# Kernel tuning notes

Hardware: AMD Instinct MI355X
Metric: run time of the kernel (lower is better)

## Reference

```python
import jax, jax.numpy as jnp
import numpy as np

B, C, H, N, K = 512, 256, 1024, 500000, 5

_PARAM_DIMS = [("w_in", C, H), ("w_h1", H, H), ("w_s2", H, H), ("w_s3", H, H),
               ("w_h2", H, H), ("w_s1o", H, H), ("w_s2o", H, H), ("w_h3", H, H),
               ("w_mu", H, C), ("w_s", H, C)]


def setup_inputs() -> dict:
    key = jax.random.key(0)
    inp = {}
    k_codes, k_book, k_params = jax.random.split(key, 3)
    inp["codes"] = jax.random.normal(k_codes, (B, C), dtype=jnp.float32)
    inp["codebook"] = jax.random.normal(k_book, (N, C), dtype=jnp.float32)
    ks = jax.random.split(k_params, len(_PARAM_DIMS))
    for (name, fin, fout), k in zip(_PARAM_DIMS, ks):
        k1, k2 = jax.random.split(k)
        s = 1.0 / np.sqrt(fin)
        inp[name] = jax.random.uniform(k1, (fout, fin), minval=-s, maxval=s, dtype=jnp.float32)
        inp["b" + name[1:]] = jax.random.uniform(k2, (fout,), minval=-s, maxval=s, dtype=jnp.float32)
    return inp


def _linear(x, w, b):
    # torch nn.Linear: x @ W^T + b, W is [out, in]
    return x @ w.T + b


def _encode(prev, w_in, b_in, w_h1, b_h1, w_s2, b_s2, w_s3, b_s3,
            w_h2, b_h2, w_s1o, b_s1o, w_s2o, b_s2o, w_h3, b_h3,
            w_mu, b_mu, w_s, b_s):
    i = jnp.tanh(_linear(prev, w_in, b_in))
    h1 = jnp.tanh(_linear(i, w_h1, b_h1))
    s2 = jnp.tanh(_linear(h1, w_s2, b_s2))
    s3 = jnp.tanh(_linear(h1, w_s3, b_s3))
    h2 = jnp.tanh(_linear(h1 + s2, w_h2, b_h2))
    o1 = jnp.tanh(_linear(h1, w_s1o, b_s1o))
    o2 = jnp.tanh(_linear(h2, w_s2o, b_s2o))
    o3 = jnp.tanh(_linear(h2 + s3, w_h3, b_h3))
    out = o1 + o2 + o3
    return _linear(out, w_mu, b_mu), _linear(out, w_s, b_s)


def reference(codes, codebook, w_in, b_in, w_h1, b_h1, w_s2, b_s2, w_s3, b_s3,
              w_h2, b_h2, w_s1o, b_s1o, w_s2o, b_s2o, w_h3, b_h3,
              w_mu, b_mu, w_s, b_s):
    # flat k-NN search: squared L2 dists via the matmul expansion
    codes2 = jnp.sum(codebook * codebook, axis=1)                      # [N]
    dists = (-2.0 * (codes @ codebook.T)
             + jnp.sum(codes * codes, axis=1, keepdims=True)
             + codes2[None, :])                                        # [B, N]
    neg_d, nbrs = jax.lax.top_k(-dists, K)                             # smallest K
    # eval mode: chosen_neighbor_index = 0 -> nearest neighbor
    prev = codebook[nbrs[:, 0]]                                        # [B, C]
    mu, logstd = _encode(prev, w_in, b_in, w_h1, b_h1, w_s2, b_s2, w_s3, b_s3,
                         w_h2, b_h2, w_s1o, b_s1o, w_s2o, b_s2o, w_h3, b_h3,
                         w_mu, b_mu, w_s, b_s)
    return (mu, logstd)
```

## Files before the change

kernel.cpp:

```cpp
#include <hip/hip_runtime.h>
#include <math.h>

#define QTOT   512
#define CDIM   256
#define HDIM   1024
#define NROWS  500000
#define NB     128
#define NTILES ((NROWS + NB - 1) / NB)
#define NPADR  (NTILES * NB)
#define LDB    264
#define DELTA  2.0f

#define C0_T   1954
#define C1_T   (NTILES - C0_T)
#define C0_R   (C0_T * NB)
#define C1_R   (C1_T * NB)

typedef short bf16x8 __attribute__((ext_vector_type(8)));
typedef float f32x4  __attribute__((ext_vector_type(4)));
typedef unsigned int u32;

__device__ __forceinline__ unsigned short bf16_rne(float f) {
  unsigned u = __float_as_uint(f);
  u += 0x7FFFu + ((u >> 16) & 1u);
  return (unsigned short)(u >> 16);
}
__device__ __forceinline__ unsigned bfp2(float a, float b) {
  return (unsigned)bf16_rne(a) | ((unsigned)bf16_rne(b) << 16);
}

__device__ __forceinline__ void gld16(const void* g, void* l) {
  __builtin_amdgcn_global_load_lds((const __attribute__((address_space(1))) u32*)g,
                                   (__attribute__((address_space(3))) u32*)l, 16, 0, 0);
}

#define FMIN_DPP(x, ctrl) do { \
    int _t = __builtin_amdgcn_update_dpp(__float_as_int(x), __float_as_int(x), (ctrl), 0xF, 0xF, false); \
    x = fminf(x, __int_as_float(_t)); } while (0)
#define FADD_DPP(x, ctrl) do { \
    int _t = __builtin_amdgcn_update_dpp(__float_as_int(x), __float_as_int(x), (ctrl), 0xF, 0xF, false); \
    x += __int_as_float(_t); } while (0)

__global__ void k_prep(const float* __restrict__ codes, unsigned short* __restrict__ a0s) {
  int q = blockIdx.x, k = threadIdx.x;
  float v = -2.0f * codes[q * CDIM + k];
  int qb = q >> 7, row = q & 127, m = row >> 4, l15 = row & 15;
  int ks = k >> 5, kin = k & 31, quad = kin >> 3, off = kin & 7;
  int lane = quad * 16 + l15;
  a0s[(((qb * 8 + m) * 8 + ks) * 64 + lane) * 8 + off] = bf16_rne(v);
}

__global__ __launch_bounds__(256) void k_conv(
    const float* __restrict__ cb, unsigned short* __restrict__ cbh,
    float* __restrict__ c2, int row0, int nrows)
{
  const int lane = threadIdx.x & 63;
  const int wid  = (blockIdx.x * 256 + threadIdx.x) >> 6;
  const int nw   = (gridDim.x * 256) >> 6;
  for (int r = wid; r < nrows; r += nw) {
    const int gr = row0 + r;
    float4 v = make_float4(0.f, 0.f, 0.f, 0.f);
    if (gr < NROWS) v = *(const float4*)(cb + (size_t)gr * CDIM + lane * 4);
    float sq = v.x * v.x + v.y * v.y + v.z * v.z + v.w * v.w;
    FADD_DPP(sq, 0xB1);
    FADD_DPP(sq, 0x4E);
    FADD_DPP(sq, 0x124);
    FADD_DPP(sq, 0x128);
    sq += __shfl_xor(sq, 16);
    sq += __shfl_xor(sq, 32);
    uint2 p; p.x = bfp2(v.x, v.y); p.y = bfp2(v.z, v.w);
    *(uint2*)((char*)cbh + (size_t)r * 512 + lane * 8) = p;
    if (lane == 0) c2[r] = (gr < NROWS) ? sq : 1e30f;
  }
}

__global__ __launch_bounds__(256, 2) void k_coarse(
    const unsigned short* __restrict__ a0s,
    const unsigned short* __restrict__ cbh,
    const float* __restrict__ c2arr,
    float* __restrict__ tileMin, int nt0)
{
  __shared__ __align__(16) unsigned short Bsh[128 * 256];
  __shared__ float c2sh[128];
  __shared__ float redf[512 * 2];

  const int tid  = threadIdx.x;
  const int lane = tid & 63;
  const int w    = tid >> 6;
  const int quad = lane >> 4;
  const int l15  = lane & 15;

  const int ntl  = blockIdx.x;
  const int ntg  = nt0 + ntl;

  const int wq = (w >> 1) * 64;
  const int wn = (w & 1) * 64;

  {
    const char* tbase = (const char*)cbh + (size_t)ntl * 65536;
#pragma unroll
    for (int i2 = 0; i2 < 16; ++i2) {
      const int i   = w * 16 + i2;
      const int row = 2 * i + (lane >> 5);
      const int cS  = lane & 31;
      gld16(tbase + (size_t)row * 512 + ((cS ^ (row & 7)) << 4),
            (char*)Bsh + i * 1024);
    }
  }
  if (tid < 128) c2sh[tid] = c2arr[ntl * NB + tid];
  __syncthreads();

  float cadd[4];
#pragma unroll
  for (int j2 = 0; j2 < 4; ++j2) cadd[j2] = c2sh[wn + j2 * 16 + l15];

  for (int qb = 0; qb < 4; ++qb) {
    const unsigned short* abase = a0s + (size_t)(qb * 8 + (w >> 1) * 4) * 4096 + lane * 8;

    f32x4 acc[4][4];
#pragma unroll
    for (int m = 0; m < 4; ++m)
#pragma unroll
      for (int j2 = 0; j2 < 4; ++j2) acc[m][j2] = (f32x4){0.f, 0.f, 0.f, 0.f};

    bf16x8 apf[3][4];
#pragma unroll
    for (int m = 0; m < 4; ++m) apf[0][m] = *(const bf16x8*)(abase + (m * 8 + 0) * 512);
#pragma unroll
    for (int m = 0; m < 4; ++m) apf[1][m] = *(const bf16x8*)(abase + (m * 8 + 1) * 512);

#pragma unroll
    for (int ks = 0; ks < 8; ++ks) {
      if (ks + 2 < 8) {
#pragma unroll
        for (int m = 0; m < 4; ++m)
          apf[(ks + 2) % 3][m] = *(const bf16x8*)(abase + (m * 8 + ks + 2) * 512);
      }
      bf16x8 b[4];
#pragma unroll
      for (int j2 = 0; j2 < 4; ++j2) {
        const int row = wn + j2 * 16 + l15;
        b[j2] = *(const bf16x8*)((const char*)Bsh + row * 512 + (((ks * 4 + quad) ^ (row & 7)) << 4));
      }
#pragma unroll
      for (int m = 0; m < 4; ++m)
#pragma unroll
        for (int j2 = 0; j2 < 4; ++j2)
          acc[m][j2] = __builtin_amdgcn_mfma_f32_16x16x32_bf16(apf[ks % 3][m], b[j2], acc[m][j2], 0, 0, 0);
    }

#pragma unroll
    for (int m = 0; m < 4; ++m) {
#pragma unroll
      for (int r = 0; r < 4; ++r) {
        float kk = fminf(fminf(acc[m][0][r] + cadd[0], acc[m][1][r] + cadd[1]),
                         fminf(acc[m][2][r] + cadd[2], acc[m][3][r] + cadd[3]));
        FMIN_DPP(kk, 0xB1);
        FMIN_DPP(kk, 0x4E);
        FMIN_DPP(kk, 0x124);
        FMIN_DPP(kk, 0x128);
        if (l15 == 0) redf[(qb * 128 + wq + m * 16 + quad * 4 + r) * 2 + (w & 1)] = kk;
      }
    }
  }
  __syncthreads();

#pragma unroll
  for (int qq = 0; qq < 2; ++qq) {
    int q = qq * 256 + tid;
    tileMin[(size_t)q * NTILES + ntg] = fminf(redf[q * 2], redf[q * 2 + 1]);
  }
}

__global__ __launch_bounds__(256, 2) void k_coarse_fb(
    const unsigned short* __restrict__ a0s,
    const float* __restrict__ cb,
    float* __restrict__ tileMin)
{
  __shared__ __align__(16) unsigned short Bsh[128 * 256];
  __shared__ float c2sh[128];
  __shared__ float redf[512 * 2];

  const int tid  = threadIdx.x;
  const int lane = tid & 63;
  const int w    = tid >> 6;
  const int quad = lane >> 4;
  const int l15  = lane & 15;

  const int nt = blockIdx.x;
  const int n0 = nt * NB;

  const int wq = (w >> 1) * 64;
  const int wn = (w & 1) * 64;

#pragma unroll 8
  for (int j = 0; j < 32; ++j) {
    int f = j * 256 + tid;
    int row = f >> 6;
    int c4  = f & 63;
    int n   = n0 + row;
    float4 v = make_float4(0.f, 0.f, 0.f, 0.f);
    if (n < NROWS) v = *(const float4*)(cb + (size_t)n * CDIM + c4 * 4);
    float sq = v.x * v.x + v.y * v.y + v.z * v.z + v.w * v.w;
    uint2 p; p.x = bfp2(v.x, v.y); p.y = bfp2(v.z, v.w);
    int chunk = (c4 >> 1) ^ (row & 7);
    *(uint2*)((char*)Bsh + row * 512 + chunk * 16 + (c4 & 1) * 8) = p;
#pragma unroll
    for (int s = 32; s; s >>= 1) sq += __shfl_xor(sq, s);
    if (lane == 0) c2sh[row] = (n < NROWS) ? sq : 1e30f;
  }
  __syncthreads();

  float cadd[4];
#pragma unroll
  for (int j2 = 0; j2 < 4; ++j2) cadd[j2] = c2sh[wn + j2 * 16 + l15];

  for (int qb = 0; qb < 4; ++qb) {
    bf16x8 afr[4][8];
    {
      const int mg0 = (w >> 1) * 4;
      const unsigned short* base = a0s + (size_t)(qb * 8 + mg0) * 8 * 64 * 8 + lane * 8;
#pragma unroll
      for (int m = 0; m < 4; ++m)
#pragma unroll
        for (int ks = 0; ks < 8; ++ks)
          afr[m][ks] = *(const bf16x8*)(base + (m * 8 + ks) * 64 * 8);
    }
    f32x4 acc[4][4];
#pragma unroll
    for (int m = 0; m < 4; ++m)
#pragma unroll
      for (int j2 = 0; j2 < 4; ++j2) acc[m][j2] = (f32x4){0.f, 0.f, 0.f, 0.f};
#pragma unroll
    for (int ks = 0; ks < 8; ++ks) {
      bf16x8 b[4];
      const int cbase = ks * 4 + quad;
#pragma unroll
      for (int j2 = 0; j2 < 4; ++j2) {
        const int row = wn + j2 * 16 + l15;
        b[j2] = *(const bf16x8*)((const char*)Bsh + row * 512 + ((cbase ^ (row & 7)) << 4));
      }
#pragma unroll
      for (int m = 0; m < 4; ++m)
#pragma unroll
        for (int j2 = 0; j2 < 4; ++j2)
          acc[m][j2] = __builtin_amdgcn_mfma_f32_16x16x32_bf16(afr[m][ks], b[j2], acc[m][j2], 0, 0, 0);
    }
#pragma unroll
    for (int m = 0; m < 4; ++m) {
#pragma unroll
      for (int r = 0; r < 4; ++r) {
        float kk = 1e30f;
#pragma unroll
        for (int j2 = 0; j2 < 4; ++j2) kk = fminf(kk, acc[m][j2][r] + cadd[j2]);
#pragma unroll
        for (int s = 1; s < 16; s <<= 1) kk = fminf(kk, __shfl_xor(kk, s));
        if (l15 == 0) redf[(qb * 128 + wq + m * 16 + quad * 4 + r) * 2 + (w & 1)] = kk;
      }
    }
  }
  __syncthreads();

#pragma unroll
  for (int qq = 0; qq < 2; ++qq) {
    int q = qq * 256 + tid;
    tileMin[(size_t)q * NTILES + nt] = fminf(redf[q * 2], redf[q * 2 + 1]);
  }
}

__global__ __launch_bounds__(256) void k_refine(
    const float* __restrict__ codes, const float* __restrict__ cb,
    const float* __restrict__ tileMin, float* __restrict__ prev)
{
#define LCAP 96
  __shared__ float csh[256];
  __shared__ float red[256];
  __shared__ int   list[LCAP];
  __shared__ int   cnt;
  __shared__ double rd[256];
  __shared__ int    rn[256];

  const int q = blockIdx.x;
  const int tid = threadIdx.x;
  csh[tid] = codes[q * CDIM + tid];
  if (tid == 0) cnt = 0;
  const float* tm = tileMin + (size_t)q * NTILES;
  float lm = 1e30f;
  for (int t = tid; t < NTILES; t += 256) lm = fminf(lm, tm[t]);
  red[tid] = lm;
  __syncthreads();
  for (int s = 128; s; s >>= 1) {
    if (tid < s) red[tid] = fminf(red[tid], red[tid + s]);
    __syncthreads();
  }
  const float thresh = red[0] + DELTA;
  for (int t = tid; t < NTILES; t += 256)
    if (tm[t] <= thresh) { int p = atomicAdd(&cnt, 1); if (p < LCAP) list[p] = t; }
  __syncthreads();
  const int nl = min(cnt, LCAP);

  double bestK = 1e300; int bestN = 0x7FFFFFFF;
  for (int li = 0; li < nl; ++li) {
    const int t = list[li];
    const int row = tid >> 1, half = tid & 1;
    const int n = t * NB + row;
    if (n < NROWS) {
      const float* r = cb + (size_t)n * CDIM;
      double dot = 0.0, sq = 0.0;
      for (int u = half * 32; u < half * 32 + 32; ++u) {
        float4 cv = *(const float4*)(r + u * 4);
        dot += (double)cv.x * csh[u*4+0] + (double)cv.y * csh[u*4+1]
             + (double)cv.z * csh[u*4+2] + (double)cv.w * csh[u*4+3];
        sq  += (double)cv.x * cv.x + (double)cv.y * cv.y
             + (double)cv.z * cv.z + (double)cv.w * cv.w;
      }
      dot += __shfl_xor(dot, 1);
      sq  += __shfl_xor(sq, 1);
      double key = sq - 2.0 * dot;
      if (key < bestK || (key == bestK && n < bestN)) { bestK = key; bestN = n; }
    }
  }
  rd[tid] = bestK; rn[tid] = bestN;
  __syncthreads();
  for (int s = 128; s; s >>= 1) {
    if (tid < s) {
      if (rd[tid + s] < rd[tid] || (rd[tid + s] == rd[tid] && rn[tid + s] < rn[tid])) {
        rd[tid] = rd[tid + s]; rn[tid] = rn[tid + s];
      }
    }
    __syncthreads();
  }
  const int nstar = rn[0];
  prev[(size_t)q * CDIM + tid] = cb[(size_t)nstar * CDIM + tid];
}

struct Job {
  const float* A1; const float* A2; const float* A3;
  const float* W;  const float* bias; float* out;
};

__global__ __launch_bounds__(256) void k_gemm(
    Job j0, Job j1, Job j2, int Kdim, int Ntot, int do_tanh)
{
  __shared__ unsigned short Ash[128 * LDB];
  __shared__ unsigned short Wsh[64 * LDB];
  __shared__ float bsh[64];

  const Job jb = (blockIdx.z == 0) ? j0 : ((blockIdx.z == 1) ? j1 : j2);
  const float* __restrict__ A1 = jb.A1;
  const float* __restrict__ A2 = jb.A2;
  const float* __restrict__ A3 = jb.A3;
  const float* __restrict__ W  = jb.W;

  const int tid  = threadIdx.x;
  const int lane = tid & 63;
  const int w    = tid >> 6;
  const int quad = lane >> 4;
  const int l15  = lane & 15;
  const int q0   = blockIdx.x * 128;
  const int n0   = blockIdx.y * 64;

  if (tid < 64) bsh[tid] = jb.bias[n0 + tid];

  f32x4 acc[2][4];
#pragma unroll
  for (int m = 0; m < 2; ++m)
#pragma unroll
    for (int j = 0; j < 4; ++j) acc[m][j] = (f32x4){0.f, 0.f, 0.f, 0.f};

  for (int kc = 0; kc < Kdim; kc += 256) {
    __syncthreads();
#pragma unroll 4
    for (int it = 0; it < 32; ++it) {
      int i = it * 256 + tid;
      int row = i >> 6, c4 = i & 63;
      size_t gi = (size_t)(q0 + row) * Kdim + kc + c4 * 4;
      float4 v = *(const float4*)(A1 + gi);
      if (A2) { float4 u = *(const float4*)(A2 + gi); v.x += u.x; v.y += u.y; v.z += u.z; v.w += u.w; }
      if (A3) { float4 u = *(const float4*)(A3 + gi); v.x += u.x; v.y += u.y; v.z += u.z; v.w += u.w; }
      uint2 p; p.x = bfp2(v.x, v.y); p.y = bfp2(v.z, v.w);
      *(uint2*)&Ash[row * LDB + c4 * 4] = p;
    }
#pragma unroll 4
    for (int it = 0; it < 16; ++it) {
      int i = it * 256 + tid;
      int row = i >> 6, c4 = i & 63;
      size_t gi = (size_t)(n0 + row) * Kdim + kc + c4 * 4;
      float4 v = *(const float4*)(W + gi);
      uint2 p; p.x = bfp2(v.x, v.y); p.y = bfp2(v.z, v.w);
      *(uint2*)&Wsh[row * LDB + c4 * 4] = p;
    }
    __syncthreads();
#pragma unroll
    for (int ks = 0; ks < 8; ++ks) {
      const int kb = ks * 32 + quad * 8;
      bf16x8 a[2], b[4];
#pragma unroll
      for (int m = 0; m < 2; ++m)
        a[m] = *(const bf16x8*)&Ash[(w * 32 + m * 16 + l15) * LDB + kb];
#pragma unroll
      for (int j = 0; j < 4; ++j)
        b[j] = *(const bf16x8*)&Wsh[(j * 16 + l15) * LDB + kb];
#pragma unroll
      for (int m = 0; m < 2; ++m)
#pragma unroll
        for (int j = 0; j < 4; ++j)
          acc[m][j] = __builtin_amdgcn_mfma_f32_16x16x32_bf16(a[m], b[j], acc[m][j], 0, 0, 0);
    }
  }

#pragma unroll
  for (int m = 0; m < 2; ++m)
#pragma unroll
    for (int j = 0; j < 4; ++j)
#pragma unroll
      for (int r = 0; r < 4; ++r) {
        int q = q0 + w * 32 + m * 16 + quad * 4 + r;
        int n = j * 16 + l15;
        float v = acc[m][j][r] + bsh[n];
        if (do_tanh) v = tanhf(v);
        jb.out[(size_t)q * Ntot + n0 + n] = v;
      }
}

extern "C" void kernel_launch(void* const* d_in, const int* in_sizes, int n_in,
                              void* d_out, int out_size, void* d_ws, size_t ws_size,
                              hipStream_t stream) {
  const float* codes = (const float*)d_in[0];
  const float* cb    = (const float*)d_in[1];
  const float* w_in  = (const float*)d_in[2];
  const float* b_in  = (const float*)d_in[3];
  const float* w_h1  = (const float*)d_in[4];
  const float* b_h1  = (const float*)d_in[5];
  const float* w_s2  = (const float*)d_in[6];
  const float* b_s2  = (const float*)d_in[7];
  const float* w_s3  = (const float*)d_in[8];
  const float* b_s3  = (const float*)d_in[9];
  const float* w_h2  = (const float*)d_in[10];
  const float* b_h2  = (const float*)d_in[11];
  const float* w_s1o = (const float*)d_in[12];
  const float* b_s1o = (const float*)d_in[13];
  const float* w_s2o = (const float*)d_in[14];
  const float* b_s2o = (const float*)d_in[15];
  const float* w_h3  = (const float*)d_in[16];
  const float* b_h3  = (const float*)d_in[17];
  const float* w_mu  = (const float*)d_in[18];
  const float* b_mu  = (const float*)d_in[19];
  const float* w_s   = (const float*)d_in[20];
  const float* b_s   = (const float*)d_in[21];
  float* out = (float*)d_out;

  char* ws = (char*)d_ws;
  unsigned short* a0s = (unsigned short*)ws;
  float* tileMin = (float*)(ws + 262144);
  float* prev    = (float*)(ws + 262144 + 8001536);
  float* acts    = (float*)(ws + 262144 + 8001536 + 524288);
  const int ACT = 512 * 1024;
  float* act_i  = acts + 0 * ACT;
  float* act_h1 = acts + 1 * ACT;
  float* act_s2 = acts + 2 * ACT;
  float* act_s3 = acts + 3 * ACT;
  float* act_h2 = acts + 4 * ACT;
  float* act_o1 = acts + 5 * ACT;
  float* act_o2 = acts + 6 * ACT;
  float* act_o3 = acts + 7 * ACT;

  const size_t CBH_OFF = 262144 + 8001536 + 524288 + 16777216;
  const size_t CBH_SZ  = (size_t)C0_R * 512;
  const size_t C2_OFF  = CBH_OFF + CBH_SZ;
  const size_t NEED    = C2_OFF + (size_t)C0_R * 4;
  unsigned short* cbh = (unsigned short*)(ws + CBH_OFF);
  float* c2buf        = (float*)(ws + C2_OFF);

  hipLaunchKernelGGL(k_prep, dim3(512), dim3(256), 0, stream, codes, a0s);

  if (ws_size >= NEED) {
    hipLaunchKernelGGL(k_conv,   dim3(2048), dim3(256), 0, stream, cb, cbh, c2buf, 0, C0_R);
    hipLaunchKernelGGL(k_coarse, dim3(C0_T), dim3(256), 0, stream, a0s, cbh, c2buf, tileMin, 0);
    hipLaunchKernelGGL(k_conv,   dim3(2048), dim3(256), 0, stream, cb, cbh, c2buf, C0_R, C1_R);
    hipLaunchKernelGGL(k_coarse, dim3(C1_T), dim3(256), 0, stream, a0s, cbh, c2buf, tileMin, C0_T);
  } else {
    hipLaunchKernelGGL(k_coarse_fb, dim3(NTILES), dim3(256), 0, stream, a0s, cb, tileMin);
  }

  hipLaunchKernelGGL(k_refine, dim3(512), dim3(256), 0, stream, codes, cb, tileMin, prev);

  const float* NUL = nullptr;
  Job in_j  = { prev,   NUL,    NUL,    w_in,  b_in,  act_i  };
  Job h1_j  = { act_i,  NUL,    NUL,    w_h1,  b_h1,  act_h1 };
  Job s2_j  = { act_h1, NUL,    NUL,    w_s2,  b_s2,  act_s2 };
  Job s3_j  = { act_h1, NUL,    NUL,    w_s3,  b_s3,  act_s3 };
  Job o1_j  = { act_h1, NUL,    NUL,    w_s1o, b_s1o, act_o1 };
  Job h2_j  = { act_h1, act_s2, NUL,    w_h2,  b_h2,  act_h2 };
  Job o2_j  = { act_h2, NUL,    NUL,    w_s2o, b_s2o, act_o2 };
  Job o3_j  = { act_h2, act_s3, NUL,    w_h3,  b_h3,  act_o3 };
  Job mu_j  = { act_o1, act_o2, act_o3, w_mu,  b_mu,  out            };
  Job ls_j  = { act_o1, act_o2, act_o3, w_s,   b_s,   out + 131072   };

  hipLaunchKernelGGL(k_gemm, dim3(4, 16, 1), dim3(256), 0, stream, in_j, in_j, in_j, 256,  1024, 1);
  hipLaunchKernelGGL(k_gemm, dim3(4, 16, 1), dim3(256), 0, stream, h1_j, h1_j, h1_j, 1024, 1024, 1);
  hipLaunchKernelGGL(k_gemm, dim3(4, 16, 3), dim3(256), 0, stream, s2_j, s3_j, o1_j, 1024, 1024, 1);
  hipLaunchKernelGGL(k_gemm, dim3(4, 16, 1), dim3(256), 0, stream, h2_j, h2_j, h2_j, 1024, 1024, 1);
  hipLaunchKernelGGL(k_gemm, dim3(4, 16, 2), dim3(256), 0, stream, o2_j, o3_j, o3_j, 1024, 1024, 1);
  hipLaunchKernelGGL(k_gemm, dim3(4, 4, 2),  dim3(256), 0, stream, mu_j, ls_j, ls_j, 1024, 256,  0);
}
```

Before: 1.332 ms.

## Persistent coarse kernel with resident query fragments and 16-row group refinement

The coarse kNN kernel becomes persistent: 256 blocks of 512 threads each keep all query A-fragments in registers and stream codebook tiles in double-buffered 64-row halves. It also records per-16-row group minima in a new workspace buffer. Refinement then rescans in fp64 only the 16-row groups under the threshold instead of whole 128-row tiles, cutting the exact rescoring work. The cost is heavy register pressure from holding 32 A fragments per thread, plus a large groupMin write (about 4000 tiles × 8 groups × 512 queries × 4 bytes) and a larger workspace requirement that may push execution onto the fallback path.

```diff
diff --git a/kernel.cpp b/kernel.cpp
--- a/kernel.cpp
+++ b/kernel.cpp
@@ -7,7 +7,7 @@
 #define NROWS  500000
 #define NB     128
 #define NTILES ((NROWS + NB - 1) / NB)
-#define NPADR  (NTILES * NB)
+#define NGRP   (NTILES * 8)
 #define LDB    264
 #define DELTA  2.0f
 
@@ -74,48 +74,76 @@
   }
 }
 
-__global__ __launch_bounds__(256, 2) void k_coarse(
+__device__ __forceinline__ void stage_half(const unsigned short* __restrict__ cbh,
+                                           int ntl, int h, unsigned short* buf,
+                                           int w, int lane) {
+  const char* tb = (const char*)cbh + (size_t)ntl * 65536 + h * 32768;
+  const int lrow0 = w * 8;
+  const int cS = lane & 31;
+  const int rpar = lane >> 5;
+#pragma unroll
+  for (int i2 = 0; i2 < 4; ++i2) {
+    const int lrow = lrow0 + i2 * 2 + rpar;
+    gld16(tb + (size_t)lrow * 512 + ((cS ^ (lrow & 7)) << 4),
+          (char*)buf + (lrow0 + i2 * 2) * 512);
+  }
+}
+
+__global__ __launch_bounds__(512, 2) void k_coarse(
     const unsigned short* __restrict__ a0s,
     const unsigned short* __restrict__ cbh,
     const float* __restrict__ c2arr,
-    float* __restrict__ tileMin, int nt0)
+    float* __restrict__ tileMin,
+    float* __restrict__ groupMin,
+    int nt0, int ctiles)
 {
-  __shared__ __align__(16) unsigned short Bsh[128 * 256];
-  __shared__ float c2sh[128];
-  __shared__ float redf[512 * 2];
+  __shared__ __align__(16) unsigned short Bsh[2][64 * 256];
+  __shared__ float c2sh[8 * 128];
+  __shared__ float hb[8][512];
 
   const int tid  = threadIdx.x;
   const int lane = tid & 63;
   const int w    = tid >> 6;
   const int quad = lane >> 4;
   const int l15  = lane & 15;
-
-  const int ntl  = blockIdx.x;
-  const int ntg  = nt0 + ntl;
-
-  const int wq = (w >> 1) * 64;
-  const int wn = (w & 1) * 64;
-
+  const int bid  = blockIdx.x;
+  const int NBL  = gridDim.x;
+
+  const int myT = (ctiles - bid + NBL - 1) / NBL;
+
+  for (int i = tid; i < myT * 128; i += 512)
+    c2sh[i] = c2arr[(bid + (i >> 7) * NBL) * 128 + (i & 127)];
+
+  bf16x8 afr[4][8];
   {
-    const char* tbase = (const char*)cbh + (size_t)ntl * 65536;
-#pragma unroll
-    for (int i2 = 0; i2 < 16; ++i2) {
-      const int i   = w * 16 + i2;
-      const int row = 2 * i + (lane >> 5);
-      const int cS  = lane & 31;
-      gld16(tbase + (size_t)row * 512 + ((cS ^ (row & 7)) << 4),
-            (char*)Bsh + i * 1024);
-    }
-  }
-  if (tid < 128) c2sh[tid] = c2arr[ntl * NB + tid];
-  __syncthreads();
-
-  float cadd[4];
-#pragma unroll
-  for (int j2 = 0; j2 < 4; ++j2) cadd[j2] = c2sh[wn + j2 * 16 + l15];
-
-  for (int qb = 0; qb < 4; ++qb) {
-    const unsigned short* abase = a0s + (size_t)(qb * 8 + (w >> 1) * 4) * 4096 + lane * 8;
+    const unsigned short* base = a0s + ((w >> 1) * 8 + (w & 1) * 4) * 4096 + lane * 8;
+#pragma unroll
+    for (int m = 0; m < 4; ++m)
+#pragma unroll
+      for (int ks = 0; ks < 8; ++ks)
+        afr[m][ks] = *(const bf16x8*)(base + (m * 8 + ks) * 512);
+  }
+
+  stage_half(cbh, bid, 0, Bsh[0], w, lane);
+  __syncthreads();
+
+  const int nh = myT * 2;
+  for (int hh = 0; hh < nh; ++hh) {
+    const int k = hh >> 1, h = hh & 1, buf = hh & 1;
+
+    if (hh + 1 < nh) {
+      stage_half(cbh, bid + ((hh + 1) >> 1) * NBL, (hh + 1) & 1, Bsh[buf ^ 1], w, lane);
+      asm volatile("s_waitcnt vmcnt(4)" ::: "memory");
+    } else {
+      asm volatile("s_waitcnt vmcnt(0)" ::: "memory");
+    }
+    __builtin_amdgcn_s_barrier();
+    __builtin_amdgcn_sched_barrier(0);
+
+    float cadd[4];
+#pragma unroll
+    for (int j2 = 0; j2 < 4; ++j2)
+      cadd[j2] = c2sh[k * 128 + h * 64 + j2 * 16 + l15];
 
     f32x4 acc[4][4];
 #pragma unroll
@@ -123,53 +151,53 @@
 #pragma unroll
       for (int j2 = 0; j2 < 4; ++j2) acc[m][j2] = (f32x4){0.f, 0.f, 0.f, 0.f};
 
-    bf16x8 apf[3][4];
-#pragma unroll
-    for (int m = 0; m < 4; ++m) apf[0][m] = *(const bf16x8*)(abase + (m * 8 + 0) * 512);
-#pragma unroll
-    for (int m = 0; m < 4; ++m) apf[1][m] = *(const bf16x8*)(abase + (m * 8 + 1) * 512);
-
 #pragma unroll
     for (int ks = 0; ks < 8; ++ks) {
-      if (ks + 2 < 8) {
-#pragma unroll
-        for (int m = 0; m < 4; ++m)
-          apf[(ks + 2) % 3][m] = *(const bf16x8*)(abase + (m * 8 + ks + 2) * 512);
-      }
       bf16x8 b[4];
 #pragma unroll
       for (int j2 = 0; j2 < 4; ++j2) {
-        const int row = wn + j2 * 16 + l15;
-        b[j2] = *(const bf16x8*)((const char*)Bsh + row * 512 + (((ks * 4 + quad) ^ (row & 7)) << 4));
+        const int lrow = j2 * 16 + l15;
+        b[j2] = *(const bf16x8*)((const char*)Bsh[buf] + lrow * 512 + (((ks * 4 + quad) ^ (lrow & 7)) << 4));
       }
 #pragma unroll
       for (int m = 0; m < 4; ++m)
 #pragma unroll
         for (int j2 = 0; j2 < 4; ++j2)
-          acc[m][j2] = __builtin_amdgcn_mfma_f32_16x16x32_bf16(apf[ks % 3][m], b[j2], acc[m][j2], 0, 0, 0);
-    }
-
+          acc[m][j2] = __builtin_amdgcn_mfma_f32_16x16x32_bf16(afr[m][ks], b[j2], acc[m][j2], 0, 0, 0);
+    }
+
+    const int ntg = nt0 + bid + k * NBL;
 #pragma unroll
     for (int m = 0; m < 4; ++m) {
 #pragma unroll
       for (int r = 0; r < 4; ++r) {
-        float kk = fminf(fminf(acc[m][0][r] + cadd[0], acc[m][1][r] + cadd[1]),
-                         fminf(acc[m][2][r] + cadd[2], acc[m][3][r] + cadd[3]));
-        FMIN_DPP(kk, 0xB1);
-        FMIN_DPP(kk, 0x4E);
-        FMIN_DPP(kk, 0x124);
-        FMIN_DPP(kk, 0x128);
-        if (l15 == 0) redf[(qb * 128 + wq + m * 16 + quad * 4 + r) * 2 + (w & 1)] = kk;
-      }
-    }
-  }
-  __syncthreads();
-
-#pragma unroll
-  for (int qq = 0; qq < 2; ++qq) {
-    int q = qq * 256 + tid;
-    tileMin[(size_t)q * NTILES + ntg] = fminf(redf[q * 2], redf[q * 2 + 1]);
-  }
+        float g4[4];
+#pragma unroll
+        for (int j2 = 0; j2 < 4; ++j2) {
+          float kk = acc[m][j2][r] + cadd[j2];
+          FMIN_DPP(kk, 0xB1);
+          FMIN_DPP(kk, 0x4E);
+          FMIN_DPP(kk, 0x124);
+          FMIN_DPP(kk, 0x128);
+          g4[j2] = kk;
+        }
+        float hmin = fminf(fminf(g4[0], g4[1]), fminf(g4[2], g4[3]));
+        if (l15 == 0) {
+          const int q = w * 64 + m * 16 + quad * 4 + r;
+#pragma unroll
+          for (int j2 = 0; j2 < 4; ++j2)
+            groupMin[(size_t)(ntg * 8 + h * 4 + j2) * 512 + q] = g4[j2];
+          hb[k][q] = h ? fminf(hb[k][q], hmin) : hmin;
+        }
+      }
+    }
+    __builtin_amdgcn_s_barrier();
+    __builtin_amdgcn_sched_barrier(0);
+  }
+
+  __syncthreads();
+  for (int k = 0; k < myT; ++k)
+    tileMin[(size_t)tid * NTILES + (nt0 + bid + k * NBL)] = hb[k][tid];
 }
 
 __global__ __launch_bounds__(256, 2) void k_coarse_fb(
@@ -270,9 +298,10 @@
 
 __global__ __launch_bounds__(256) void k_refine(
     const float* __restrict__ codes, const float* __restrict__ cb,
-    const float* __restrict__ tileMin, float* __restrict__ prev)
+    const float* __restrict__ tileMin, const float* __restrict__ groupMin,
+    float* __restrict__ prev)
 {
-#define LCAP 96
+#define LCAP 256
   __shared__ float csh[256];
   __shared__ float red[256];
   __shared__ int   list[LCAP];
@@ -294,30 +323,68 @@
     __syncthreads();
   }
   const float thresh = red[0] + DELTA;
-  for (int t = tid; t < NTILES; t += 256)
-    if (tm[t] <= thresh) { int p = atomicAdd(&cnt, 1); if (p < LCAP) list[p] = t; }
+
+  if (groupMin) {
+    for (int t = tid; t < NTILES; t += 256)
+      if (tm[t] <= thresh) {
+#pragma unroll
+        for (int g = 0; g < 8; ++g) {
+          float gv = groupMin[(size_t)(t * 8 + g) * 512 + q];
+          if (gv <= thresh) { int p = atomicAdd(&cnt, 1); if (p < LCAP) list[p] = t * 8 + g; }
+        }
+      }
+  } else {
+    for (int t = tid; t < NTILES; t += 256)
+      if (tm[t] <= thresh) { int p = atomicAdd(&cnt, 1); if (p < LCAP) list[p] = t; }
+  }
   __syncthreads();
   const int nl = min(cnt, LCAP);
 
   double bestK = 1e300; int bestN = 0x7FFFFFFF;
-  for (int li = 0; li < nl; ++li) {
-    const int t = list[li];
-    const int row = tid >> 1, half = tid & 1;
-    const int n = t * NB + row;
-    if (n < NROWS) {
-      const float* r = cb + (size_t)n * CDIM;
-      double dot = 0.0, sq = 0.0;
-      for (int u = half * 32; u < half * 32 + 32; ++u) {
-        float4 cv = *(const float4*)(r + u * 4);
-        dot += (double)cv.x * csh[u*4+0] + (double)cv.y * csh[u*4+1]
-             + (double)cv.z * csh[u*4+2] + (double)cv.w * csh[u*4+3];
-        sq  += (double)cv.x * cv.x + (double)cv.y * cv.y
-             + (double)cv.z * cv.z + (double)cv.w * cv.w;
-      }
-      dot += __shfl_xor(dot, 1);
-      sq  += __shfl_xor(sq, 1);
-      double key = sq - 2.0 * dot;
-      if (key < bestK || (key == bestK && n < bestN)) { bestK = key; bestN = n; }
+  if (groupMin) {
+    for (int li = 0; li < nl; li += 8) {
+      const int idx = li + (tid >> 5);
+      if (idx < nl) {
+        const int grp = list[idx];
+        const int rowin = (tid >> 1) & 15, half = tid & 1;
+        const int n = grp * 16 + rowin;
+        if (n < NROWS) {
+          const float* r = cb + (size_t)n * CDIM;
+          double dot = 0.0, sq = 0.0;
+          for (int u = half * 32; u < half * 32 + 32; ++u) {
+            float4 cv = *(const float4*)(r + u * 4);
+            dot += (double)cv.x * csh[u*4+0] + (double)cv.y * csh[u*4+1]
+                 + (double)cv.z * csh[u*4+2] + (double)cv.w * csh[u*4+3];
+            sq  += (double)cv.x * cv.x + (double)cv.y * cv.y
+                 + (double)cv.z * cv.z + (double)cv.w * cv.w;
+          }
+          dot += __shfl_xor(dot, 1);
+          sq  += __shfl_xor(sq, 1);
+          double key = sq - 2.0 * dot;
+          if (key < bestK || (key == bestK && n < bestN)) { bestK = key; bestN = n; }
+        }
+      }
+    }
+  } else {
+    for (int li = 0; li < nl; ++li) {
+      const int t = list[li];
+      const int row = tid >> 1, half = tid & 1;
+      const int n = t * NB + row;
+      if (n < NROWS) {
+        const float* r = cb + (size_t)n * CDIM;
+        double dot = 0.0, sq = 0.0;
+        for (int u = half * 32; u < half * 32 + 32; ++u) {
+          float4 cv = *(const float4*)(r + u * 4);
+          dot += (double)cv.x * csh[u*4+0] + (double)cv.y * csh[u*4+1]
+               + (double)cv.z * csh[u*4+2] + (double)cv.w * csh[u*4+3];
+          sq  += (double)cv.x * cv.x + (double)cv.y * cv.y
+               + (double)cv.z * cv.z + (double)cv.w * cv.w;
+        }
+        dot += __shfl_xor(dot, 1);
+        sq  += __shfl_xor(sq, 1);
+        double key = sq - 2.0 * dot;
+        if (key < bestK || (key == bestK && n < bestN)) { bestK = key; bestN = n; }
+      }
     }
   }
   rd[tid] = bestK; rn[tid] = bestN;
@@ -468,22 +535,28 @@
   const size_t CBH_OFF = 262144 + 8001536 + 524288 + 16777216;
   const size_t CBH_SZ  = (size_t)C0_R * 512;
   const size_t C2_OFF  = CBH_OFF + CBH_SZ;
-  const size_t NEED    = C2_OFF + (size_t)C0_R * 4;
+  const size_t C2_SZ   = (size_t)C0_R * 4;
+  const size_t GM_OFF  = C2_OFF + C2_SZ;
+  const size_t GM_SZ   = (size_t)NGRP * 512 * 4;
+  const size_t NEED    = GM_OFF + GM_SZ;
   unsigned short* cbh = (unsigned short*)(ws + CBH_OFF);
   float* c2buf        = (float*)(ws + C2_OFF);
+  float* gmin         = (float*)(ws + GM_OFF);
 
   hipLaunchKernelGGL(k_prep, dim3(512), dim3(256), 0, stream, codes, a0s);
 
-  if (ws_size >= NEED) {
+  bool use_groups = (ws_size >= NEED);
+  if (use_groups) {
     hipLaunchKernelGGL(k_conv,   dim3(2048), dim3(256), 0, stream, cb, cbh, c2buf, 0, C0_R);
-    hipLaunchKernelGGL(k_coarse, dim3(C0_T), dim3(256), 0, stream, a0s, cbh, c2buf, tileMin, 0);
+    hipLaunchKernelGGL(k_coarse, dim3(256),  dim3(512), 0, stream, a0s, cbh, c2buf, tileMin, gmin, 0, C0_T);
     hipLaunchKernelGGL(k_conv,   dim3(2048), dim3(256), 0, stream, cb, cbh, c2buf, C0_R, C1_R);
-    hipLaunchKernelGGL(k_coarse, dim3(C1_T), dim3(256), 0, stream, a0s, cbh, c2buf, tileMin, C0_T);
+    hipLaunchKernelGGL(k_coarse, dim3(256),  dim3(512), 0, stream, a0s, cbh, c2buf, tileMin, gmin, C0_T, C1_T);
   } else {
     hipLaunchKernelGGL(k_coarse_fb, dim3(NTILES), dim3(256), 0, stream, a0s, cb, tileMin);
   }
 
-  hipLaunchKernelGGL(k_refine, dim3(512), dim3(256), 0, stream, codes, cb, tileMin, prev);
+  hipLaunchKernelGGL(k_refine, dim3(512), dim3(256), 0, stream, codes, cb, tileMin,
+                     use_groups ? gmin : (const float*)nullptr, prev);
 
   const float* NUL = nullptr;
   Job in_j  = { prev,   NUL,    NUL,    w_in,  b_in,  act_i  };
```

Result: slower. 1.436 ms (+7.9%).
